# Kernel tuning notes

Hardware: AMD Instinct MI355X
Metric: run time of the kernel (lower is better)

## Reference

```python
import jax, jax.numpy as jnp
import numpy as np

N_NODES = 100_000
N_EDGES = 1_600_000
F_IN = 128
NHID = 128
G = 64            # num graphs in the batch
N_CLASSES = 2
EMB = NHID * 6    # embedding_data dim so concat dim == NHID*8


def _lin_init(k, fi, fo):
    s = 1.0 / np.sqrt(fi)
    k1, k2 = jax.random.split(k)
    w = jax.random.uniform(k1, (fi, fo), jnp.float32, -s, s)
    b = jax.random.uniform(k2, (fo,), jnp.float32, -s, s)
    return w, b


def setup_inputs() -> dict:
    key = jax.random.key(0)
    ks = jax.random.split(key, 12)
    x = jax.random.normal(ks[0], (N_NODES, F_IN), jnp.float32)
    edge_index = jax.random.randint(ks[1], (2, N_EDGES), 0, N_NODES, dtype=jnp.int32)
    per = N_NODES // G
    batch = jnp.minimum(jnp.arange(N_NODES, dtype=jnp.int32) // per, G - 1)  # sorted, even split
    embedding_data = jax.random.normal(ks[2], (G, EMB), jnp.float32)
    conv_w, conv_b = _lin_init(ks[3], F_IN, NHID)
    lin0_w, lin0_b = _lin_init(ks[4], F_IN, NHID)
    lin1_w, lin1_b = _lin_init(ks[5], NHID * 8, NHID * 4)
    lin2_w, lin2_b = _lin_init(ks[6], NHID * 4, NHID * 2)
    lin3_w, lin3_b = _lin_init(ks[7], NHID * 2, NHID)
    lin4_w, lin4_b = _lin_init(ks[8], NHID, N_CLASSES)
    return {
        "x": x, "embedding_data": embedding_data,
        "conv_w": conv_w, "conv_b": conv_b,
        "lin0_w": lin0_w, "lin0_b": lin0_b,
        "lin1_w": lin1_w, "lin1_b": lin1_b,
        "lin2_w": lin2_w, "lin2_b": lin2_b,
        "lin3_w": lin3_w, "lin3_b": lin3_b,
        "lin4_w": lin4_w, "lin4_b": lin4_b,
        "edge_index": edge_index, "batch": batch,
    }


def _gcn_conv(x, edge_index, w, b):
    """PyG GCNConv: add self-loops, symmetric deg^-1/2 normalization, linear, scatter-add."""
    n = x.shape[0]
    loop = jnp.arange(n, dtype=edge_index.dtype)
    src = jnp.concatenate([edge_index[0], loop])
    dst = jnp.concatenate([edge_index[1], loop])
    deg = jax.ops.segment_sum(jnp.ones_like(dst, dtype=x.dtype), dst, num_segments=n)
    dinv = jnp.where(deg > 0, jax.lax.rsqrt(deg), 0.0)
    norm = dinv[src] * dinv[dst]                     # [E+N]
    h = x @ w                                        # [N, NHID]
    msg = h[src] * norm[:, None]                     # gather  [E+N, NHID]
    out = jax.ops.segment_sum(msg, dst, num_segments=n)  # scatter-add
    return out + b


def reference(x, embedding_data, conv_w, conv_b, lin0_w, lin0_b,
              lin1_w, lin1_b, lin2_w, lin2_b, lin3_w, lin3_b,
              lin4_w, lin4_b, edge_index, batch):
    h = jax.nn.relu(_gcn_conv(x, edge_index, conv_w, conv_b))   # [N, NHID]
    pooled = jax.ops.segment_max(h, batch, num_segments=G)      # global max pool [G, NHID]
    # first node of each graph (batch is sorted)
    first_idx = jnp.searchsorted(batch, jnp.arange(G, dtype=batch.dtype))
    news = jax.nn.relu(x[first_idx] @ lin0_w + lin0_b)          # [G, NHID]
    z = jnp.concatenate([pooled, news, embedding_data], axis=1) # [G, NHID*8]
    z = jnp.tanh(z @ lin1_w + lin1_b)   # dropout = identity (eval mode)
    z = jnp.tanh(z @ lin2_w + lin2_b)
    z = jnp.tanh(z @ lin3_w + lin3_b)
    return jax.nn.log_softmax(z @ lin4_w + lin4_b, axis=-1)     # [G, N_CLASSES]
```

## Files before the change

kernel.cpp:

```cpp
#include <hip/hip_runtime.h>
#include <hip/hip_bf16.h>

#define N_NODES 100000
#define N_EDGES 1600000
#define F 128
#define G 64
#define EMB 768
#define PER 1562
#define CAP 96
#define NBUCK 256
#define BNODES 391
#define TILE 8192
#define NBIN 196
#define SLOT 80
#define GEMM_GRID 512
#define EWS_STRIDE 98

typedef __hip_bfloat16 bf16;
typedef __attribute__((ext_vector_type(8))) short short8;
typedef __attribute__((ext_vector_type(4))) float f32x4;
typedef unsigned int u32;

__device__ __forceinline__ float b2f(bf16 v) { return __bfloat162float(v); }
__device__ __forceinline__ short f2bs(float v) {
    bf16 b = __float2bfloat16(v);
    return *reinterpret_cast<short*>(&b);
}
__device__ __forceinline__ float bl16(u32 v) { return __uint_as_float(v << 16); }
__device__ __forceinline__ float bh16(u32 v) { return __uint_as_float(v & 0xffff0000u); }

__global__ void k_init(float* __restrict__ pooled) {
    int i = blockIdx.x * 256 + threadIdx.x;
    if (i < G * F) pooled[i] = 0.0f;
}

__global__ __launch_bounds__(256) void k_fat(const int* __restrict__ ei,
                                             int* __restrict__ cntarr,
                                             u32* __restrict__ stage,
                                             const float* __restrict__ x,
                                             const float* __restrict__ w,
                                             bf16* __restrict__ h) {
    int t = threadIdx.x;
    if (blockIdx.x < NBIN) {
        __shared__ int offs[NBUCK];
        offs[t] = 0;
        __syncthreads();
        int blk = blockIdx.x;
        int e0 = blk * TILE;
        int e1 = min(e0 + TILE, N_EDGES);
        for (int e = e0 + t; e < e1; e += 256) {
            int src = ei[e];
            int dst = ei[N_EDGES + e];
            int b = dst / BNODES;
            int dl = dst - b * BNODES;
            int pos = atomicAdd(&offs[b], 1);
            if (pos < SLOT)
                stage[((size_t)b * NBIN + blk) * SLOT + pos] = (u32)src | ((u32)dl << 17);
        }
        __syncthreads();
        cntarr[blk * NBUCK + t] = min(offs[t], SLOT);
    } else {
        __shared__ short wfrag[16384];
        for (int i = t; i < 16384; i += 256) {
            int j    = i & 7;
            int lane = (i >> 3) & 63;
            int kb   = (i >> 9) & 3;
            int ct   = i >> 11;
            int k    = kb * 32 + (lane >> 4) * 8 + j;
            int n    = ct * 16 + (lane & 15);
            wfrag[i] = f2bs(w[k * 128 + n]);
        }
        __syncthreads();

        int wv = t >> 6, lane = t & 63;
        int m = lane & 15, q = lane >> 4;
        int nchunks = (N_NODES + 63) / 64;
        for (int chunk = blockIdx.x - NBIN; chunk < nchunks; chunk += GEMM_GRID) {
            int row = chunk * 64 + wv * 16 + m;
            int rr = (row < N_NODES) ? row : 0;
            short8 a[4];
#pragma unroll
            for (int kb = 0; kb < 4; ++kb) {
                const float* src = x + (size_t)rr * F + kb * 32 + q * 8;
                float4 v0 = *(const float4*)src;
                float4 v1 = *(const float4*)(src + 4);
                short8 av;
                av[0] = f2bs(v0.x); av[1] = f2bs(v0.y); av[2] = f2bs(v0.z); av[3] = f2bs(v0.w);
                av[4] = f2bs(v1.x); av[5] = f2bs(v1.y); av[6] = f2bs(v1.z); av[7] = f2bs(v1.w);
                a[kb] = av;
            }
            f32x4 acc[8];
#pragma unroll
            for (int ct = 0; ct < 8; ++ct) {
                f32x4 c = {0.f, 0.f, 0.f, 0.f};
#pragma unroll
                for (int kb = 0; kb < 4; ++kb) {
                    short8 bfr = *(const short8*)&wfrag[((ct * 4 + kb) * 64 + lane) * 8];
                    c = __builtin_amdgcn_mfma_f32_16x16x32_bf16(a[kb], bfr, c, 0, 0, 0);
                }
                acc[ct] = c;
            }
            int rbase = chunk * 64 + wv * 16 + q * 4;
#pragma unroll
            for (int ct = 0; ct < 8; ++ct)
#pragma unroll
                for (int r = 0; r < 4; ++r) {
                    int ro = rbase + r;
                    if (ro < N_NODES) h[(size_t)ro * F + ct * 16 + m] = __float2bfloat16(acc[ct][r]);
                }
        }
    }
}

__global__ __launch_bounds__(1024) void k_scat(const u32* __restrict__ stage,
                                               const int* __restrict__ cntarr,
                                               int* __restrict__ cursor,
                                               float* __restrict__ dinv,
                                               int* __restrict__ slots) {
    __shared__ int lcur[BNODES];
    int b = blockIdx.x;
    int t = threadIdx.x;
    int wv = t >> 6, lane = t & 63;
    int nbase = b * BNODES;
    int bn = min(BNODES, N_NODES - nbase);
    if (bn <= 0) return;
    for (int l = t; l < bn; l += 1024) lcur[l] = 0;
    __syncthreads();
    for (int seg = wv; seg < NBIN; seg += 16) {
        int cnt = cntarr[seg * NBUCK + b];
        const u32* sp = stage + ((size_t)b * NBIN + seg) * SLOT;
        for (int i = lane; i < cnt; i += 64) {
            u32 p = sp[i];
            int src = (int)(p & 0x1FFFFu);
            int dl  = (int)(p >> 17);
            int pos = atomicAdd(&lcur[dl], 1);
            if (pos < CAP) slots[(size_t)(nbase + dl) * CAP + pos] = src;
        }
    }
    __syncthreads();
    for (int l = t; l < bn; l += 1024) {
        int c = lcur[l];
        cursor[nbase + l] = c;
        dinv[nbase + l] = rsqrtf((float)(c + 1));
    }
}

__global__ __launch_bounds__(256) void k_agg(const bf16* __restrict__ h,
                                             const float* __restrict__ dinv,
                                             const int* __restrict__ slots,
                                             const int* __restrict__ cnt,
                                             const float* __restrict__ cb,
                                             float* __restrict__ pooled) {
    __shared__ __align__(16) char smem[16 * EWS_STRIDE * 8];
    int2 (*ews)[EWS_STRIDE] = (int2(*)[EWS_STRIDE])smem;
    float (*red)[132] = (float(*)[132])smem;

    int t = threadIdx.x;
    int wv = t >> 6, lane = t & 63;
    int q  = lane >> 4;
    int fl = lane & 15;
    int nb = blockIdx.x * 16 + wv * 4;
    int node = nb + q;
    int row  = wv * 4 + q;

    int c0 = min(cnt[nb + 0], CAP), c1 = min(cnt[nb + 1], CAP);
    int c2 = min(cnt[nb + 2], CAP), c3 = min(cnt[nb + 3], CAP);
    int cq   = (q == 0) ? c0 : (q == 1) ? c1 : (q == 2) ? c2 : c3;
    int cmax = max(max(c0, c1), max(c2, c3));

    const int* slp = slots + (size_t)node * CAP;
#pragma unroll
    for (int k = 0; k < 6; ++k) {
        int j = k * 16 + fl;
        int2 ew = {0, 0};
        if (j < cq) { int s = slp[j]; ew.x = s; ew.y = __float_as_int(dinv[s]); }
        ews[row][j] = ew;
    }
    __syncthreads();

    float acc[8] = {0.f, 0.f, 0.f, 0.f, 0.f, 0.f, 0.f, 0.f};
    const uint4* ewv = (const uint4*)ews[row];
    const u32* hb = (const u32*)h;
    int fl4 = fl * 4;
    for (int s0 = 0; s0 < cmax; s0 += 4) {
        uint4 ea = ewv[(s0 >> 1) + 0];
        uint4 eb = ewv[(s0 >> 1) + 1];
        uint4 v0 = *(const uint4*)(hb + (size_t)ea.x * 64 + fl4);
        uint4 v1 = *(const uint4*)(hb + (size_t)ea.z * 64 + fl4);
        uint4 v2 = *(const uint4*)(hb + (size_t)eb.x * 64 + fl4);
        uint4 v3 = *(const uint4*)(hb + (size_t)eb.z * 64 + fl4);
        float w0 = __uint_as_float(ea.y), w1 = __uint_as_float(ea.w);
        float w2 = __uint_as_float(eb.y), w3 = __uint_as_float(eb.w);
        acc[0] = fmaf(bl16(v0.x), w0, acc[0]);
        acc[1] = fmaf(bh16(v0.x), w0, acc[1]);
        acc[2] = fmaf(bl16(v0.y), w0, acc[2]);
        acc[3] = fmaf(bh16(v0.y), w0, acc[3]);
        acc[4] = fmaf(bl16(v0.z), w0, acc[4]);
        acc[5] = fmaf(bh16(v0.z), w0, acc[5]);
        acc[6] = fmaf(bl16(v0.w), w0, acc[6]);
        acc[7] = fmaf(bh16(v0.w), w0, acc[7]);
        acc[0] = fmaf(bl16(v1.x), w1, acc[0]);
        acc[1] = fmaf(bh16(v1.x), w1, acc[1]);
        acc[2] = fmaf(bl16(v1.y), w1, acc[2]);
        acc[3] = fmaf(bh16(v1.y), w1, acc[3]);
        acc[4] = fmaf(bl16(v1.z), w1, acc[4]);
        acc[5] = fmaf(bh16(v1.z), w1, acc[5]);
        acc[6] = fmaf(bl16(v1.w), w1, acc[6]);
        acc[7] = fmaf(bh16(v1.w), w1, acc[7]);
        acc[0] = fmaf(bl16(v2.x), w2, acc[0]);
        acc[1] = fmaf(bh16(v2.x), w2, acc[1]);
        acc[2] = fmaf(bl16(v2.y), w2, acc[2]);
        acc[3] = fmaf(bh16(v2.y), w2, acc[3]);
        acc[4] = fmaf(bl16(v2.z), w2, acc[4]);
        acc[5] = fmaf(bh16(v2.z), w2, acc[5]);
        acc[6] = fmaf(bl16(v2.w), w2, acc[6]);
        acc[7] = fmaf(bh16(v2.w), w2, acc[7]);
        acc[0] = fmaf(bl16(v3.x), w3, acc[0]);
        acc[1] = fmaf(bh16(v3.x), w3, acc[1]);
        acc[2] = fmaf(bl16(v3.y), w3, acc[2]);
        acc[3] = fmaf(bh16(v3.y), w3, acc[3]);
        acc[4] = fmaf(bl16(v3.z), w3, acc[4]);
        acc[5] = fmaf(bh16(v3.z), w3, acc[5]);
        acc[6] = fmaf(bl16(v3.w), w3, acc[6]);
        acc[7] = fmaf(bh16(v3.w), w3, acc[7]);
    }

    float dn = dinv[node];
    float dn2 = dn * dn;
    uint4 hs = *(const uint4*)(hb + (size_t)node * 64 + fl4);
    float4 cbv0 = *(const float4*)&cb[8 * fl];
    float4 cbv1 = *(const float4*)&cb[8 * fl + 4];
    float s0v = fmaxf(fmaf(acc[0], dn, fmaf(bl16(hs.x), dn2, cbv0.x)), 0.f);
    float s1v = fmaxf(fmaf(acc[1], dn, fmaf(bh16(hs.x), dn2, cbv0.y)), 0.f);
    float s2v = fmaxf(fmaf(acc[2], dn, fmaf(bl16(hs.y), dn2, cbv0.z)), 0.f);
    float s3v = fmaxf(fmaf(acc[3], dn, fmaf(bh16(hs.y), dn2, cbv0.w)), 0.f);
    float s4v = fmaxf(fmaf(acc[4], dn, fmaf(bl16(hs.z), dn2, cbv1.x)), 0.f);
    float s5v = fmaxf(fmaf(acc[5], dn, fmaf(bh16(hs.z), dn2, cbv1.y)), 0.f);
    float s6v = fmaxf(fmaf(acc[6], dn, fmaf(bl16(hs.w), dn2, cbv1.z)), 0.f);
    float s7v = fmaxf(fmaf(acc[7], dn, fmaf(bh16(hs.w), dn2, cbv1.w)), 0.f);

    __syncthreads();
    *(float4*)&red[row][8 * fl]     = make_float4(s0v, s1v, s2v, s3v);
    *(float4*)&red[row][8 * fl + 4] = make_float4(s4v, s5v, s6v, s7v);
    __syncthreads();

    int n0 = blockIdx.x * 16;
    int g0 = min(n0 / PER, G - 1);
    int gL = min((n0 + 15) / PER, G - 1);
    if (g0 == gL) {
        if (wv == 0) {
            float m0 = red[0][2 * lane], m1 = red[0][2 * lane + 1];
#pragma unroll
            for (int r = 1; r < 16; ++r) {
                m0 = fmaxf(m0, red[r][2 * lane]);
                m1 = fmaxf(m1, red[r][2 * lane + 1]);
            }
            atomicMax((int*)&pooled[g0 * F + 2 * lane],     __float_as_int(m0));
            atomicMax((int*)&pooled[g0 * F + 2 * lane + 1], __float_as_int(m1));
        }
    } else {
#pragma unroll
        for (int r = 0; r < 4; ++r) {
            int rr = wv * 4 + r;
            int g = min((n0 + rr) / PER, G - 1);
            atomicMax((int*)&pooled[g * F + 2 * lane],     __float_as_int(red[rr][2 * lane]));
            atomicMax((int*)&pooled[g * F + 2 * lane + 1], __float_as_int(red[rr][2 * lane + 1]));
        }
    }
}

__global__ __launch_bounds__(256) void k_l1(const float* __restrict__ x,
                                            const float* __restrict__ pooled,
                                            const float* __restrict__ emb,
                                            const float* __restrict__ l0w,
                                            const float* __restrict__ l0b,
                                            const float* __restrict__ w1,
                                            const float* __restrict__ b1,
                                            float* __restrict__ z1) {
    int g = blockIdx.x >> 3, jc = blockIdx.x & 7;
    int t = threadIdx.x;
    __shared__ float zs[1024];
    __shared__ float xs[128];
    __shared__ float psum[4][64];
    if (t < 128) {
        xs[t] = x[(size_t)(g * PER) * F + t];
        zs[t] = pooled[g * 128 + t];
    }
    for (int i = t; i < EMB; i += 256) zs[256 + i] = emb[g * EMB + i];
    __syncthreads();
    if (t < 128) {
        float acc = l0b[t];
        for (int k = 0; k < 128; ++k) acc += xs[k] * l0w[k * 128 + t];
        zs[128 + t] = fmaxf(acc, 0.f);
    }
    __syncthreads();
    int j = t & 63, kc = t >> 6;
    float acc = 0.f;
    const float* wp = w1 + (size_t)(kc * 256) * 512 + jc * 64 + j;
#pragma unroll 4
    for (int k = 0; k < 256; ++k)
        acc += zs[kc * 256 + k] * wp[(size_t)k * 512];
    psum[kc][j] = acc;
    __syncthreads();
    if (t < 64) {
        float s = b1[jc * 64 + t] + psum[0][t] + psum[1][t] + psum[2][t] + psum[3][t];
        z1[g * 512 + jc * 64 + t] = tanhf(s);
    }
}

__global__ __launch_bounds__(256) void k_l2(const float* __restrict__ z1,
                                            const float* __restrict__ w2,
                                            const float* __restrict__ b2,
                                            float* __restrict__ z2) {
    int g = blockIdx.x >> 2, jc = blockIdx.x & 3;
    int t = threadIdx.x, j = t & 63, kc = t >> 6;
    __shared__ float zs[512];
    __shared__ float psum[4][64];
    for (int i = t; i < 512; i += 256) zs[i] = z1[g * 512 + i];
    __syncthreads();
    float acc = 0.f;
    const float* wp = w2 + (size_t)(kc * 128) * 256 + jc * 64 + j;
#pragma unroll 4
    for (int k = 0; k < 128; ++k)
        acc += zs[kc * 128 + k] * wp[(size_t)k * 256];
    psum[kc][j] = acc;
    __syncthreads();
    if (t < 64) {
        float s = b2[jc * 64 + t] + psum[0][t] + psum[1][t] + psum[2][t] + psum[3][t];
        z2[g * 256 + jc * 64 + t] = tanhf(s);
    }
}

__global__ __launch_bounds__(256) void k_l3out(const float* __restrict__ z2,
                                               const float* __restrict__ w3,
                                               const float* __restrict__ b3,
                                               const float* __restrict__ w4,
                                               const float* __restrict__ b4,
                                               float* __restrict__ out) {
    int g = blockIdx.x, t = threadIdx.x;
    __shared__ float zs[256];
    __shared__ float psum[2][128];
    __shared__ float z3s[128];
    zs[t] = z2[g * 256 + t];
    __syncthreads();
    int j = t & 127, kc = t >> 7;
    float acc = 0.f;
    const float* wp = w3 + (size_t)(kc * 128) * 128 + j;
#pragma unroll 4
    for (int k = 0; k < 128; ++k)
        acc += zs[kc * 128 + k] * wp[(size_t)k * 128];
    psum[kc][j] = acc;
    __syncthreads();
    if (t < 128) z3s[t] = tanhf(b3[t] + psum[0][t] + psum[1][t]);
    __syncthreads();
    if (t < 2) {
        float l = b4[t];
        for (int k = 0; k < 128; ++k) l += z3s[k] * w4[k * 2 + t];
        psum[0][t] = l;
    }
    __syncthreads();
    if (t == 0) {
        float l0 = psum[0][0], l1 = psum[0][1];
        float m = fmaxf(l0, l1);
        float lse = m + logf(expf(l0 - m) + expf(l1 - m));
        out[g * 2 + 0] = l0 - lse;
        out[g * 2 + 1] = l1 - lse;
    }
}

extern "C" void kernel_launch(void* const* d_in, const int* in_sizes, int n_in,
                              void* d_out, int out_size, void* d_ws, size_t ws_size,
                              hipStream_t stream) {
    const float* x      = (const float*)d_in[0];
    const float* emb    = (const float*)d_in[1];
    const float* conv_w = (const float*)d_in[2];
    const float* conv_b = (const float*)d_in[3];
    const float* lin0_w = (const float*)d_in[4];
    const float* lin0_b = (const float*)d_in[5];
    const float* lin1_w = (const float*)d_in[6];
    const float* lin1_b = (const float*)d_in[7];
    const float* lin2_w = (const float*)d_in[8];
    const float* lin2_b = (const float*)d_in[9];
    const float* lin3_w = (const float*)d_in[10];
    const float* lin3_b = (const float*)d_in[11];
    const float* lin4_w = (const float*)d_in[12];
    const float* lin4_b = (const float*)d_in[13];
    const int*   ei     = (const int*)d_in[14];
    float* out = (float*)d_out;

    char* ws = (char*)d_ws;
    int*   cursor = (int*)ws;                         ws += (size_t)N_NODES * 4;
    float* dinv   = (float*)ws;                       ws += (size_t)N_NODES * 4;
    int*   slots  = (int*)ws;                         ws += (size_t)N_NODES * CAP * 4;
    bf16*  h      = (bf16*)ws;                        ws += (size_t)N_NODES * F * 2;
    float* pooled = (float*)ws;                       ws += (size_t)G * F * 4;
    int*   cntarr = (int*)ws;                         ws += (size_t)NBIN * NBUCK * 4;
    u32*   stage  = (u32*)ws;                         ws += (size_t)NBUCK * NBIN * SLOT * 4;
    float* z1     = (float*)ws;                       ws += (size_t)G * 512 * 4;
    float* z2     = (float*)ws;                       ws += (size_t)G * 256 * 4;

    k_init<<<(G * F + 255) / 256, 256, 0, stream>>>(pooled);
    k_fat<<<NBIN + GEMM_GRID, 256, 0, stream>>>(ei, cntarr, stage, x, conv_w, h);
    k_scat<<<NBUCK, 1024, 0, stream>>>(stage, cntarr, cursor, dinv, slots);
    k_agg<<<N_NODES / 16, 256, 0, stream>>>(h, dinv, slots, cursor, conv_b, pooled);
    k_l1<<<G * 8, 256, 0, stream>>>(x, pooled, emb, lin0_w, lin0_b, lin1_w, lin1_b, z1);
    k_l2<<<G * 4, 256, 0, stream>>>(z1, lin2_w, lin2_b, z2);
    k_l3out<<<G, 256, 0, stream>>>(z2, lin3_w, lin3_b, lin4_w, lin4_b, out);
}
```

Before: 309.8 us.

## Software-pipeline neighbor gathers in aggregation and batch 8 graphs per MLP block

```diff
diff --git a/kernel.cpp b/kernel.cpp
--- a/kernel.cpp
+++ b/kernel.cpp
@@ -14,7 +14,7 @@
 #define NBIN 196
 #define SLOT 80
 #define GEMM_GRID 512
-#define EWS_STRIDE 98
+#define EWS_ENT 104
 
 typedef __hip_bfloat16 bf16;
 typedef __attribute__((ext_vector_type(8))) short short8;
@@ -151,8 +151,8 @@
                                              const int* __restrict__ cnt,
                                              const float* __restrict__ cb,
                                              float* __restrict__ pooled) {
-    __shared__ __align__(16) char smem[16 * EWS_STRIDE * 8];
-    int2 (*ews)[EWS_STRIDE] = (int2(*)[EWS_STRIDE])smem;
+    __shared__ __align__(16) char smem[16 * EWS_ENT * 8];
+    int2 (*ews)[EWS_ENT] = (int2(*)[EWS_ENT])smem;
     float (*red)[132] = (float(*)[132])smem;
 
     int t = threadIdx.x;
@@ -170,11 +170,13 @@
 
     const int* slp = slots + (size_t)node * CAP;
 #pragma unroll
-    for (int k = 0; k < 6; ++k) {
+    for (int k = 0; k < 7; ++k) {
         int j = k * 16 + fl;
-        int2 ew = {0, 0};
-        if (j < cq) { int s = slp[j]; ew.x = s; ew.y = __float_as_int(dinv[s]); }
-        ews[row][j] = ew;
+        if (j < EWS_ENT) {
+            int2 ew = {0, 0};
+            if (j < cq) { int s = slp[j]; ew.x = s; ew.y = __float_as_int(dinv[s]); }
+            ews[row][j] = ew;
+        }
     }
     __syncthreads();
 
@@ -182,47 +184,57 @@
     const uint4* ewv = (const uint4*)ews[row];
     const u32* hb = (const u32*)h;
     int fl4 = fl * 4;
-    for (int s0 = 0; s0 < cmax; s0 += 4) {
-        uint4 ea = ewv[(s0 >> 1) + 0];
-        uint4 eb = ewv[(s0 >> 1) + 1];
+    if (cmax > 0) {
+        uint4 ea = ewv[0];
+        uint4 eb = ewv[1];
         uint4 v0 = *(const uint4*)(hb + (size_t)ea.x * 64 + fl4);
         uint4 v1 = *(const uint4*)(hb + (size_t)ea.z * 64 + fl4);
         uint4 v2 = *(const uint4*)(hb + (size_t)eb.x * 64 + fl4);
         uint4 v3 = *(const uint4*)(hb + (size_t)eb.z * 64 + fl4);
-        float w0 = __uint_as_float(ea.y), w1 = __uint_as_float(ea.w);
-        float w2 = __uint_as_float(eb.y), w3 = __uint_as_float(eb.w);
-        acc[0] = fmaf(bl16(v0.x), w0, acc[0]);
-        acc[1] = fmaf(bh16(v0.x), w0, acc[1]);
-        acc[2] = fmaf(bl16(v0.y), w0, acc[2]);
-        acc[3] = fmaf(bh16(v0.y), w0, acc[3]);
-        acc[4] = fmaf(bl16(v0.z), w0, acc[4]);
-        acc[5] = fmaf(bh16(v0.z), w0, acc[5]);
-        acc[6] = fmaf(bl16(v0.w), w0, acc[6]);
-        acc[7] = fmaf(bh16(v0.w), w0, acc[7]);
-        acc[0] = fmaf(bl16(v1.x), w1, acc[0]);
-        acc[1] = fmaf(bh16(v1.x), w1, acc[1]);
-        acc[2] = fmaf(bl16(v1.y), w1, acc[2]);
-        acc[3] = fmaf(bh16(v1.y), w1, acc[3]);
-        acc[4] = fmaf(bl16(v1.z), w1, acc[4]);
-        acc[5] = fmaf(bh16(v1.z), w1, acc[5]);
-        acc[6] = fmaf(bl16(v1.w), w1, acc[6]);
-        acc[7] = fmaf(bh16(v1.w), w1, acc[7]);
-        acc[0] = fmaf(bl16(v2.x), w2, acc[0]);
-        acc[1] = fmaf(bh16(v2.x), w2, acc[1]);
-        acc[2] = fmaf(bl16(v2.y), w2, acc[2]);
-        acc[3] = fmaf(bh16(v2.y), w2, acc[3]);
-        acc[4] = fmaf(bl16(v2.z), w2, acc[4]);
-        acc[5] = fmaf(bh16(v2.z), w2, acc[5]);
-        acc[6] = fmaf(bl16(v2.w), w2, acc[6]);
-        acc[7] = fmaf(bh16(v2.w), w2, acc[7]);
-        acc[0] = fmaf(bl16(v3.x), w3, acc[0]);
-        acc[1] = fmaf(bh16(v3.x), w3, acc[1]);
-        acc[2] = fmaf(bl16(v3.y), w3, acc[2]);
-        acc[3] = fmaf(bh16(v3.y), w3, acc[3]);
-        acc[4] = fmaf(bl16(v3.z), w3, acc[4]);
-        acc[5] = fmaf(bh16(v3.z), w3, acc[5]);
-        acc[6] = fmaf(bl16(v3.w), w3, acc[6]);
-        acc[7] = fmaf(bh16(v3.w), w3, acc[7]);
+        for (int s0 = 0; s0 < cmax; s0 += 4) {
+            uint4 na = ewv[(s0 >> 1) + 2];
+            uint4 nb4 = ewv[(s0 >> 1) + 3];
+            uint4 n0 = *(const uint4*)(hb + (size_t)na.x * 64 + fl4);
+            uint4 n1 = *(const uint4*)(hb + (size_t)na.z * 64 + fl4);
+            uint4 n2 = *(const uint4*)(hb + (size_t)nb4.x * 64 + fl4);
+            uint4 n3 = *(const uint4*)(hb + (size_t)nb4.z * 64 + fl4);
+            float w0 = __uint_as_float(ea.y), w1 = __uint_as_float(ea.w);
+            float w2 = __uint_as_float(eb.y), w3 = __uint_as_float(eb.w);
+            acc[0] = fmaf(bl16(v0.x), w0, acc[0]);
+            acc[1] = fmaf(bh16(v0.x), w0, acc[1]);
+            acc[2] = fmaf(bl16(v0.y), w0, acc[2]);
+            acc[3] = fmaf(bh16(v0.y), w0, acc[3]);
+            acc[4] = fmaf(bl16(v0.z), w0, acc[4]);
+            acc[5] = fmaf(bh16(v0.z), w0, acc[5]);
+            acc[6] = fmaf(bl16(v0.w), w0, acc[6]);
+            acc[7] = fmaf(bh16(v0.w), w0, acc[7]);
+            acc[0] = fmaf(bl16(v1.x), w1, acc[0]);
+            acc[1] = fmaf(bh16(v1.x), w1, acc[1]);
+            acc[2] = fmaf(bl16(v1.y), w1, acc[2]);
+            acc[3] = fmaf(bh16(v1.y), w1, acc[3]);
+            acc[4] = fmaf(bl16(v1.z), w1, acc[4]);
+            acc[5] = fmaf(bh16(v1.z), w1, acc[5]);
+            acc[6] = fmaf(bl16(v1.w), w1, acc[6]);
+            acc[7] = fmaf(bh16(v1.w), w1, acc[7]);
+            acc[0] = fmaf(bl16(v2.x), w2, acc[0]);
+            acc[1] = fmaf(bh16(v2.x), w2, acc[1]);
+            acc[2] = fmaf(bl16(v2.y), w2, acc[2]);
+            acc[3] = fmaf(bh16(v2.y), w2, acc[3]);
+            acc[4] = fmaf(bl16(v2.z), w2, acc[4]);
+            acc[5] = fmaf(bh16(v2.z), w2, acc[5]);
+            acc[6] = fmaf(bl16(v2.w), w2, acc[6]);
+            acc[7] = fmaf(bh16(v2.w), w2, acc[7]);
+            acc[0] = fmaf(bl16(v3.x), w3, acc[0]);
+            acc[1] = fmaf(bh16(v3.x), w3, acc[1]);
+            acc[2] = fmaf(bl16(v3.y), w3, acc[2]);
+            acc[3] = fmaf(bh16(v3.y), w3, acc[3]);
+            acc[4] = fmaf(bl16(v3.z), w3, acc[4]);
+            acc[5] = fmaf(bh16(v3.z), w3, acc[5]);
+            acc[6] = fmaf(bl16(v3.w), w3, acc[6]);
+            acc[7] = fmaf(bh16(v3.w), w3, acc[7]);
+            ea = na; eb = nb4;
+            v0 = n0; v1 = n1; v2 = n2; v3 = n3;
+        }
     }
 
     float dn = dinv[node];
@@ -277,34 +289,52 @@
                                             const float* __restrict__ w1,
                                             const float* __restrict__ b1,
                                             float* __restrict__ z1) {
-    int g = blockIdx.x >> 3, jc = blockIdx.x & 7;
-    int t = threadIdx.x;
-    __shared__ float zs[1024];
-    __shared__ float xs[128];
-    __shared__ float psum[4][64];
+    int jc = blockIdx.x & 7;
+    int g0 = (blockIdx.x >> 3) * 8;
+    int t = threadIdx.x;
+    __shared__ float zs[8][1024];
+    __shared__ float xs[8][128];
+    __shared__ float psum[4][8][64];
+    for (int i = t; i < 8 * 128; i += 256) {
+        int g = i >> 7, c = i & 127;
+        zs[g][c] = pooled[(g0 + g) * 128 + c];
+        xs[g][c] = x[(size_t)((g0 + g) * PER) * F + c];
+    }
+    for (int i = t; i < 8 * 768; i += 256) {
+        int g = i / 768, c = i - g * 768;
+        zs[g][256 + c] = emb[(g0 + g) * EMB + c];
+    }
+    __syncthreads();
     if (t < 128) {
-        xs[t] = x[(size_t)(g * PER) * F + t];
-        zs[t] = pooled[g * 128 + t];
-    }
-    for (int i = t; i < EMB; i += 256) zs[256 + i] = emb[g * EMB + i];
-    __syncthreads();
-    if (t < 128) {
-        float acc = l0b[t];
-        for (int k = 0; k < 128; ++k) acc += xs[k] * l0w[k * 128 + t];
-        zs[128 + t] = fmaxf(acc, 0.f);
-    }
-    __syncthreads();
-    int j = t & 63, kc = t >> 6;
-    float acc = 0.f;
-    const float* wp = w1 + (size_t)(kc * 256) * 512 + jc * 64 + j;
-#pragma unroll 4
-    for (int k = 0; k < 256; ++k)
-        acc += zs[kc * 256 + k] * wp[(size_t)k * 512];
-    psum[kc][j] = acc;
-    __syncthreads();
-    if (t < 64) {
-        float s = b1[jc * 64 + t] + psum[0][t] + psum[1][t] + psum[2][t] + psum[3][t];
-        z1[g * 512 + jc * 64 + t] = tanhf(s);
+        float nacc[8];
+#pragma unroll
+        for (int g = 0; g < 8; ++g) nacc[g] = l0b[t];
+        for (int k = 0; k < 128; ++k) {
+            float lw = l0w[k * 128 + t];
+#pragma unroll
+            for (int g = 0; g < 8; ++g) nacc[g] = fmaf(xs[g][k], lw, nacc[g]);
+        }
+#pragma unroll
+        for (int g = 0; g < 8; ++g) zs[g][128 + t] = fmaxf(nacc[g], 0.f);
+    }
+    __syncthreads();
+    int j = t & 63, kq = t >> 6;
+    float acc[8] = {0.f, 0.f, 0.f, 0.f, 0.f, 0.f, 0.f, 0.f};
+    const float* wp = w1 + (size_t)(kq * 256) * 512 + jc * 64 + j;
+    for (int k = 0; k < 256; ++k) {
+        float wv = wp[(size_t)k * 512];
+        int kk = kq * 256 + k;
+#pragma unroll
+        for (int g = 0; g < 8; ++g) acc[g] = fmaf(zs[g][kk], wv, acc[g]);
+    }
+#pragma unroll
+    for (int g = 0; g < 8; ++g) psum[kq][g][j] = acc[g];
+    __syncthreads();
+    for (int i = t; i < 512; i += 256) {
+        int g = i >> 6, jj = i & 63;
+        float s = b1[jc * 64 + jj] + psum[0][g][jj] + psum[1][g][jj]
+                + psum[2][g][jj] + psum[3][g][jj];
+        z1[(g0 + g) * 512 + jc * 64 + jj] = tanhf(s);
     }
 }
 
@@ -312,22 +342,33 @@
                                             const float* __restrict__ w2,
                                             const float* __restrict__ b2,
                                             float* __restrict__ z2) {
-    int g = blockIdx.x >> 2, jc = blockIdx.x & 3;
-    int t = threadIdx.x, j = t & 63, kc = t >> 6;
-    __shared__ float zs[512];
-    __shared__ float psum[4][64];
-    for (int i = t; i < 512; i += 256) zs[i] = z1[g * 512 + i];
-    __syncthreads();
-    float acc = 0.f;
-    const float* wp = w2 + (size_t)(kc * 128) * 256 + jc * 64 + j;
-#pragma unroll 4
-    for (int k = 0; k < 128; ++k)
-        acc += zs[kc * 128 + k] * wp[(size_t)k * 256];
-    psum[kc][j] = acc;
-    __syncthreads();
-    if (t < 64) {
-        float s = b2[jc * 64 + t] + psum[0][t] + psum[1][t] + psum[2][t] + psum[3][t];
-        z2[g * 256 + jc * 64 + t] = tanhf(s);
+    int jc = blockIdx.x & 3;
+    int g0 = (blockIdx.x >> 2) * 8;
+    int t = threadIdx.x;
+    __shared__ float zs[8][512];
+    __shared__ float psum[4][8][64];
+    for (int i = t; i < 8 * 512; i += 256) {
+        int g = i >> 9, c = i & 511;
+        zs[g][c] = z1[(g0 + g) * 512 + c];
+    }
+    __syncthreads();
+    int j = t & 63, kq = t >> 6;
+    float acc[8] = {0.f, 0.f, 0.f, 0.f, 0.f, 0.f, 0.f, 0.f};
+    const float* wp = w2 + (size_t)(kq * 128) * 256 + jc * 64 + j;
+    for (int k = 0; k < 128; ++k) {
+        float wv = wp[(size_t)k * 256];
+        int kk = kq * 128 + k;
+#pragma unroll
+        for (int g = 0; g < 8; ++g) acc[g] = fmaf(zs[g][kk], wv, acc[g]);
+    }
+#pragma unroll
+    for (int g = 0; g < 8; ++g) psum[kq][g][j] = acc[g];
+    __syncthreads();
+    for (int i = t; i < 512; i += 256) {
+        int g = i >> 6, jj = i & 63;
+        float s = b2[jc * 64 + jj] + psum[0][g][jj] + psum[1][g][jj]
+                + psum[2][g][jj] + psum[3][g][jj];
+        z2[(g0 + g) * 256 + jc * 64 + jj] = tanhf(s);
     }
 }
 
@@ -337,34 +378,47 @@
                                                const float* __restrict__ w4,
                                                const float* __restrict__ b4,
                                                float* __restrict__ out) {
-    int g = blockIdx.x, t = threadIdx.x;
-    __shared__ float zs[256];
-    __shared__ float psum[2][128];
-    __shared__ float z3s[128];
-    zs[t] = z2[g * 256 + t];
-    __syncthreads();
-    int j = t & 127, kc = t >> 7;
-    float acc = 0.f;
-    const float* wp = w3 + (size_t)(kc * 128) * 128 + j;
-#pragma unroll 4
-    for (int k = 0; k < 128; ++k)
-        acc += zs[kc * 128 + k] * wp[(size_t)k * 128];
-    psum[kc][j] = acc;
-    __syncthreads();
-    if (t < 128) z3s[t] = tanhf(b3[t] + psum[0][t] + psum[1][t]);
-    __syncthreads();
-    if (t < 2) {
-        float l = b4[t];
-        for (int k = 0; k < 128; ++k) l += z3s[k] * w4[k * 2 + t];
-        psum[0][t] = l;
-    }
-    __syncthreads();
-    if (t == 0) {
-        float l0 = psum[0][0], l1 = psum[0][1];
+    int g0 = blockIdx.x * 8;
+    int t = threadIdx.x;
+    __shared__ float zs[8][256];
+    __shared__ float psum[2][8][128];
+    __shared__ float z3s[8][128];
+    __shared__ float logits[16];
+    for (int i = t; i < 8 * 256; i += 256) {
+        int g = i >> 8, c = i & 255;
+        zs[g][c] = z2[(g0 + g) * 256 + c];
+    }
+    __syncthreads();
+    int j = t & 127, kh = t >> 7;
+    float acc[8] = {0.f, 0.f, 0.f, 0.f, 0.f, 0.f, 0.f, 0.f};
+    const float* wp = w3 + (size_t)(kh * 128) * 128 + j;
+    for (int k = 0; k < 128; ++k) {
+        float wv = wp[(size_t)k * 128];
+        int kk = kh * 128 + k;
+#pragma unroll
+        for (int g = 0; g < 8; ++g) acc[g] = fmaf(zs[g][kk], wv, acc[g]);
+    }
+#pragma unroll
+    for (int g = 0; g < 8; ++g) psum[kh][g][j] = acc[g];
+    __syncthreads();
+    for (int i = t; i < 8 * 128; i += 256) {
+        int g = i >> 7, jj = i & 127;
+        z3s[g][jj] = tanhf(b3[jj] + psum[0][g][jj] + psum[1][g][jj]);
+    }
+    __syncthreads();
+    if (t < 16) {
+        int g = t >> 1, c = t & 1;
+        float l = b4[c];
+        for (int k = 0; k < 128; ++k) l += z3s[g][k] * w4[k * 2 + c];
+        logits[t] = l;
+    }
+    __syncthreads();
+    if (t < 8) {
+        float l0 = logits[2 * t], l1 = logits[2 * t + 1];
         float m = fmaxf(l0, l1);
         float lse = m + logf(expf(l0 - m) + expf(l1 - m));
-        out[g * 2 + 0] = l0 - lse;
-        out[g * 2 + 1] = l1 - lse;
+        out[(g0 + t) * 2 + 0] = l0 - lse;
+        out[(g0 + t) * 2 + 1] = l1 - lse;
     }
 }
 
@@ -403,7 +457,7 @@
     k_fat<<<NBIN + GEMM_GRID, 256, 0, stream>>>(ei, cntarr, stage, x, conv_w, h);
     k_scat<<<NBUCK, 1024, 0, stream>>>(stage, cntarr, cursor, dinv, slots);
     k_agg<<<N_NODES / 16, 256, 0, stream>>>(h, dinv, slots, cursor, conv_b, pooled);
-    k_l1<<<G * 8, 256, 0, stream>>>(x, pooled, emb, lin0_w, lin0_b, lin1_w, lin1_b, z1);
-    k_l2<<<G * 4, 256, 0, stream>>>(z1, lin2_w, lin2_b, z2);
-    k_l3out<<<G, 256, 0, stream>>>(z2, lin3_w, lin3_b, lin4_w, lin4_b, out);
-}
+    k_l1<<<64, 256, 0, stream>>>(x, pooled, emb, lin0_w, lin0_b, lin1_w, lin1_b, z1);
+    k_l2<<<32, 256, 0, stream>>>(z1, lin2_w, lin2_b, z2);
+    k_l3out<<<8, 256, 0, stream>>>(z2, lin3_w, lin3_b, lin4_w, lin4_b, out);
+}
```

Result: no change. 306.3 us (-1.1%).
